# Kernel tuning notes

Hardware: AMD Instinct MI355X
Metric: run time of the kernel (lower is better)

The kernel has to match this reference:

```python
import jax, jax.numpy as jnp
import numpy as np

N = 100000   # num_nodes
D = 128      # hidden_dim
E = 640000   # num_edges


def setup_inputs() -> dict:
    key = jax.random.key(0)
    k0, k1, k2, k3 = jax.random.split(key, 4)
    node_features = jax.random.normal(k0, (N, D), dtype=jnp.float32) * 0.02
    # GCNConv linear weights (glorot-style scale), bias initialized to zero
    scale = 1.0 / np.sqrt(D)
    W1 = jax.random.normal(k1, (D, D), dtype=jnp.float32) * scale
    b1 = jnp.zeros((D,), dtype=jnp.float32)
    W2 = jax.random.normal(k2, (D, D), dtype=jnp.float32) * scale
    b2 = jnp.zeros((D,), dtype=jnp.float32)
    edge_index = jax.random.randint(k3, (2, E), 0, N, dtype=jnp.int32)
    return {"node_features": node_features, "W1": W1, "b1": b1,
            "W2": W2, "b2": b2, "edge_index": edge_index}


def gcn_layer(x, W, b, row, col):
    # PyG GCNConv: linear (no bias) -> symmetric norm deg^-1/2 -> scatter-add -> +bias
    x = x @ W.T                                   # [N, D]
    ones = jnp.ones(row.shape, dtype=x.dtype)
    deg = jax.ops.segment_sum(ones, col, num_segments=N)   # in-degree incl. self-loops
    dis = jnp.where(deg > 0, jax.lax.rsqrt(deg), 0.0)       # deg_inv_sqrt, inf -> 0
    norm = dis[row] * dis[col]                    # [E_tot]
    msgs = norm[:, None] * x[row]                 # gather + scale, [E_tot, D]
    out = jax.ops.segment_sum(msgs, col, num_segments=N)    # scatter-aggregate
    return out + b


def reference(node_features, W1, b1, W2, b2, edge_index):
    # add self-loops once (GCNConv does this per call; same result since graph is static)
    loops = jnp.arange(N, dtype=edge_index.dtype)
    row = jnp.concatenate([edge_index[0], loops])
    col = jnp.concatenate([edge_index[1], loops])
    x = jax.nn.relu(gcn_layer(node_features, W1, b1, row, col))
    x = jax.nn.relu(gcn_layer(x, W2, b2, row, col))
    return x
```

## Files before the change

### kernel.cpp

```cpp
#include <hip/hip_runtime.h>

#define DD 128

typedef short bf16x8 __attribute__((ext_vector_type(8)));
typedef float f32x4 __attribute__((ext_vector_type(4)));

__device__ __forceinline__ unsigned short f2bf(float f) {
    unsigned int u = __builtin_bit_cast(unsigned int, f);
    u += 0x7fffu + ((u >> 16) & 1u);
    return (unsigned short)(u >> 16);
}
__device__ __forceinline__ float bflo(unsigned int u) { return __builtin_bit_cast(float, u << 16); }
__device__ __forceinline__ float bfhi(unsigned int u) { return __builtin_bit_cast(float, u & 0xffff0000u); }

__global__ __launch_bounds__(256) void k_part(const int* __restrict__ cnt,
                                              int* __restrict__ part, int n) {
    __shared__ int s[256];
    int t = threadIdx.x;
    int i = blockIdx.x * 256 + t;
    s[t] = (i < n) ? cnt[i] : 0;
    __syncthreads();
    for (int off = 128; off > 0; off >>= 1) {
        if (t < off) s[t] += s[t + off];
        __syncthreads();
    }
    if (t == 0) part[blockIdx.x] = s[0];
}

__global__ __launch_bounds__(1024) void k_scanpart(int* __restrict__ part, int nblk) {
    __shared__ int s[1024];
    int t = threadIdx.x;
    int v = (t < nblk) ? part[t] : 0;
    s[t] = v;
    __syncthreads();
    for (int off = 1; off < 1024; off <<= 1) {
        int u = (t >= off) ? s[t - off] : 0;
        __syncthreads();
        s[t] += u;
        __syncthreads();
    }
    if (t < nblk) part[t] = s[t] - v;
}

__global__ __launch_bounds__(256) void k_apply(const int* __restrict__ cnt,
                                               const int* __restrict__ part,
                                               int* __restrict__ rowptr,
                                               int* __restrict__ cursor,
                                               float* __restrict__ dis, int n) {
    __shared__ int s[256];
    int t = threadIdx.x;
    int i = blockIdx.x * 256 + t;
    int c = (i < n) ? cnt[i] : 0;
    s[t] = c;
    __syncthreads();
    for (int off = 1; off < 256; off <<= 1) {
        int u = (t >= off) ? s[t - off] : 0;
        __syncthreads();
        s[t] += u;
        __syncthreads();
    }
    int base = part[blockIdx.x] + s[t] - c;
    if (i < n) {
        rowptr[i] = base;
        cursor[i] = base;
        dis[i] = rsqrtf((float)c + 1.0f);
        if (i == n - 1) rowptr[n] = base + c;
    }
}

__global__ void k_permute(const int* __restrict__ row, const int* __restrict__ col,
                          int* __restrict__ cursor, int* __restrict__ srow, int E) {
    int e = blockIdx.x * blockDim.x + threadIdx.x;
    if (e >= E) return;
    int p = atomicAdd(&cursor[col[e]], 1);
    srow[p] = row[e];
}

template <bool INBF16, bool FUSE_COUNT>
__global__ __launch_bounds__(256) void k_gemm_mfma(const void* __restrict__ Xv,
                                                   const float* __restrict__ W,
                                                   unsigned short* __restrict__ Y,
                                                   int nrows, int gemm_blocks,
                                                   const int* __restrict__ col,
                                                   int* __restrict__ cnt, int E) {
    __shared__ unsigned short Ws[128 * 128];
    const int t = threadIdx.x;

    if (FUSE_COUNT && blockIdx.x >= gemm_blocks) {
        int e = (blockIdx.x - gemm_blocks) * 256 + t;
        if (e < E) atomicAdd(&cnt[col[e]], 1);
        return;
    }

    #pragma unroll
    for (int i = 0; i < 8; ++i) {
        int g   = i * 256 + t;
        int row = g >> 4, ch = g & 15;
        const float* src = W + row * 128 + ch * 8;
        float4 f0 = *(const float4*)src;
        float4 f1 = *(const float4*)(src + 4);
        unsigned short u[8] = { f2bf(f0.x), f2bf(f0.y), f2bf(f0.z), f2bf(f0.w),
                                f2bf(f1.x), f2bf(f1.y), f2bf(f1.z), f2bf(f1.w) };
        int dst = row * 128 + ((ch ^ (row & 15)) << 3);
        *(uint4*)&Ws[dst] = *(const uint4*)u;
    }
    __syncthreads();

    const int wid  = t >> 6;
    const int lane = t & 63;
    const int lr   = lane & 15;
    const int lk   = lane >> 4;
    const long r0  = (long)blockIdx.x * 64 + wid * 16;

    long arow = r0 + lr;
    if (arow >= nrows) arow = nrows - 1;

    f32x4 acc[8] = {};

    #pragma unroll
    for (int kc = 0; kc < 4; ++kc) {
        bf16x8 af;
        if (INBF16) {
            const unsigned short* ap = (const unsigned short*)Xv + arow * 128 + kc * 32 + lk * 8;
            af = *(const bf16x8*)ap;
        } else {
            const float* ap = (const float*)Xv + arow * 128 + kc * 32 + lk * 8;
            float4 a0 = *(const float4*)ap;
            float4 a1 = *(const float4*)(ap + 4);
            af[0] = (short)f2bf(a0.x); af[1] = (short)f2bf(a0.y);
            af[2] = (short)f2bf(a0.z); af[3] = (short)f2bf(a0.w);
            af[4] = (short)f2bf(a1.x); af[5] = (short)f2bf(a1.y);
            af[6] = (short)f2bf(a1.z); af[7] = (short)f2bf(a1.w);
        }
        #pragma unroll
        for (int jt = 0; jt < 8; ++jt) {
            int j  = jt * 16 + lr;
            int ch = (kc * 4 + lk) ^ lr;
            const bf16x8* bp = (const bf16x8*)&Ws[j * 128 + (ch << 3)];
            acc[jt] = __builtin_amdgcn_mfma_f32_16x16x32_bf16(af, *bp, acc[jt], 0, 0, 0);
        }
    }

    #pragma unroll
    for (int jt = 0; jt < 8; ++jt) {
        #pragma unroll
        for (int r = 0; r < 4; ++r) {
            long m = r0 + lk * 4 + r;
            if (m < nrows) Y[m * 128 + jt * 16 + lr] = f2bf(acc[jt][r]);
        }
    }
}

__device__ __forceinline__ void fma8(float* acc, float nm, uint4 q) {
    acc[0] += nm * bflo(q.x); acc[1] += nm * bfhi(q.x);
    acc[2] += nm * bflo(q.y); acc[3] += nm * bfhi(q.y);
    acc[4] += nm * bflo(q.z); acc[5] += nm * bfhi(q.z);
    acc[6] += nm * bflo(q.w); acc[7] += nm * bfhi(q.w);
}

template <bool OUTBF16>
__global__ __launch_bounds__(256) void k_agg(const int* __restrict__ rowptr,
                                             const int* __restrict__ srow,
                                             const float* __restrict__ dis,
                                             const unsigned short* __restrict__ xw,
                                             const float* __restrict__ b,
                                             void* __restrict__ outv, int n) {
    int v = blockIdx.x * 16 + (threadIdx.x >> 4);
    if (v >= n) return;
    int c = (threadIdx.x & 15) * 8;

    float dv = dis[v], s = dv * dv;
    float acc[8] = {};
    fma8(acc, s, *(const uint4*)(xw + (long)v * 128 + c));

    int e0 = rowptr[v], e1 = rowptr[v + 1];
    int e = e0;
    for (; e + 2 <= e1; e += 2) {
        int   r1 = srow[e],  r2 = srow[e + 1];
        float n1 = dis[r1] * dv, n2 = dis[r2] * dv;
        uint4 q1 = *(const uint4*)(xw + (long)r1 * 128 + c);
        uint4 q2 = *(const uint4*)(xw + (long)r2 * 128 + c);
        fma8(acc, n1, q1);
        fma8(acc, n2, q2);
    }
    if (e < e1) {
        int   r1 = srow[e];
        float n1 = dis[r1] * dv;
        fma8(acc, n1, *(const uint4*)(xw + (long)r1 * 128 + c));
    }

    float4 b0 = *(const float4*)(b + c);
    float4 b1 = *(const float4*)(b + c + 4);
    float o[8];
    o[0] = fmaxf(acc[0] + b0.x, 0.0f); o[1] = fmaxf(acc[1] + b0.y, 0.0f);
    o[2] = fmaxf(acc[2] + b0.z, 0.0f); o[3] = fmaxf(acc[3] + b0.w, 0.0f);
    o[4] = fmaxf(acc[4] + b1.x, 0.0f); o[5] = fmaxf(acc[5] + b1.y, 0.0f);
    o[6] = fmaxf(acc[6] + b1.z, 0.0f); o[7] = fmaxf(acc[7] + b1.w, 0.0f);

    if (OUTBF16) {
        unsigned int p[4];
        p[0] = (unsigned int)f2bf(o[0]) | ((unsigned int)f2bf(o[1]) << 16);
        p[1] = (unsigned int)f2bf(o[2]) | ((unsigned int)f2bf(o[3]) << 16);
        p[2] = (unsigned int)f2bf(o[4]) | ((unsigned int)f2bf(o[5]) << 16);
        p[3] = (unsigned int)f2bf(o[6]) | ((unsigned int)f2bf(o[7]) << 16);
        *(uint4*)((unsigned short*)outv + (long)v * 128 + c) = *(const uint4*)p;
    } else {
        float* op = (float*)outv + (long)v * 128 + c;
        *(float4*)op       = make_float4(o[0], o[1], o[2], o[3]);
        *(float4*)(op + 4) = make_float4(o[4], o[5], o[6], o[7]);
    }
}

extern "C" void kernel_launch(void* const* d_in, const int* in_sizes, int n_in,
                              void* d_out, int out_size, void* d_ws, size_t ws_size,
                              hipStream_t stream) {
    const float* X  = (const float*)d_in[0];
    const float* W1 = (const float*)d_in[1];
    const float* b1 = (const float*)d_in[2];
    const float* W2 = (const float*)d_in[3];
    const float* b2 = (const float*)d_in[4];
    const int*   ei = (const int*)d_in[5];
    const int N = in_sizes[0] / DD;
    const int E = in_sizes[5] / 2;
    const int* row = ei;
    const int* col = ei + E;

    char* p = (char*)d_ws;
    auto carve = [&](size_t bytes) { char* q = p; p += (bytes + 255) & ~(size_t)255; return q; };
    int*            cnt    = (int*)           carve((size_t)N * 4);
    int*            rowptr = (int*)           carve((size_t)(N + 1) * 4);
    int*            cursor = (int*)           carve((size_t)N * 4);
    int*            part   = (int*)           carve(1024 * 4);
    int*            srow   = (int*)           carve((size_t)E * 4);
    float*          dis    = (float*)         carve((size_t)N * 4);
    unsigned short* xw     = (unsigned short*)carve((size_t)N * DD * 2);
    unsigned short* h1     = (unsigned short*)d_out;

    const int B = 256;
    const int NBLK = (N + 255) / 256;
    const int gemm_grid  = (N + 63) / 64;
    const int count_grid = (E + B - 1) / B;
    const int agg_grid   = (N + 15) / 16;

    hipMemsetAsync(cnt, 0, (size_t)N * 4, stream);
    k_gemm_mfma<false, true><<<gemm_grid + count_grid, B, 0, stream>>>(
        X, W1, xw, N, gemm_grid, col, cnt, E);

    k_part<<<NBLK, B, 0, stream>>>(cnt, part, N);
    k_scanpart<<<1, 1024, 0, stream>>>(part, NBLK);
    k_apply<<<NBLK, B, 0, stream>>>(cnt, part, rowptr, cursor, dis, N);
    k_permute<<<count_grid, B, 0, stream>>>(row, col, cursor, srow, E);

    k_agg<true><<<agg_grid, B, 0, stream>>>(rowptr, srow, dis, xw, b1, h1, N);

    k_gemm_mfma<true, false><<<gemm_grid, B, 0, stream>>>(
        h1, W2, xw, N, gemm_grid, nullptr, nullptr, 0);
    k_agg<false><<<agg_grid, B, 0, stream>>>(rowptr, srow, dis, xw, b2, d_out, N);
}
```

Before: 175.3 us.

## Enlarge GEMM blocks, swap MFMA operands for vector stores, unroll aggregation by four

The GEMM kernel now runs 512 threads per block covering 128 rows, so the bf16 conversion of W into shared memory is spread over more rows. The MFMA operands are swapped so each lane holds four consecutive output columns of a single row, which lets the epilogue write packed 8-byte stores instead of scattered 2-byte stores. The aggregation loop is unrolled to four edges to keep more gathers in flight, with a scalar loop for the remainder. Larger blocks can cut occupancy, and the extra registers from the unroll may limit waves.

```diff
diff --git a/kernel.cpp b/kernel.cpp
--- a/kernel.cpp
+++ b/kernel.cpp
@@ -77,7 +77,7 @@
 }
 
 template <bool INBF16, bool FUSE_COUNT>
-__global__ __launch_bounds__(256) void k_gemm_mfma(const void* __restrict__ Xv,
+__global__ __launch_bounds__(512) void k_gemm_mfma(const void* __restrict__ Xv,
                                                    const float* __restrict__ W,
                                                    unsigned short* __restrict__ Y,
                                                    int nrows, int gemm_blocks,
@@ -87,14 +87,14 @@
     const int t = threadIdx.x;
 
     if (FUSE_COUNT && blockIdx.x >= gemm_blocks) {
-        int e = (blockIdx.x - gemm_blocks) * 256 + t;
+        int e = (blockIdx.x - gemm_blocks) * 512 + t;
         if (e < E) atomicAdd(&cnt[col[e]], 1);
         return;
     }
 
     #pragma unroll
-    for (int i = 0; i < 8; ++i) {
-        int g   = i * 256 + t;
+    for (int i = 0; i < 4; ++i) {
+        int g   = i * 512 + t;
         int row = g >> 4, ch = g & 15;
         const float* src = W + row * 128 + ch * 8;
         float4 f0 = *(const float4*)src;
@@ -110,10 +110,11 @@
     const int lane = t & 63;
     const int lr   = lane & 15;
     const int lk   = lane >> 4;
-    const long r0  = (long)blockIdx.x * 64 + wid * 16;
+    const long r0  = (long)blockIdx.x * 128 + wid * 16;
 
     long arow = r0 + lr;
-    if (arow >= nrows) arow = nrows - 1;
+    bool rowok = arow < nrows;
+    if (!rowok) arow = nrows - 1;
 
     f32x4 acc[8] = {};
 
@@ -137,16 +138,18 @@
             int j  = jt * 16 + lr;
             int ch = (kc * 4 + lk) ^ lr;
             const bf16x8* bp = (const bf16x8*)&Ws[j * 128 + (ch << 3)];
-            acc[jt] = __builtin_amdgcn_mfma_f32_16x16x32_bf16(af, *bp, acc[jt], 0, 0, 0);
+            acc[jt] = __builtin_amdgcn_mfma_f32_16x16x32_bf16(*bp, af, acc[jt], 0, 0, 0);
         }
     }
 
-    #pragma unroll
-    for (int jt = 0; jt < 8; ++jt) {
+    if (rowok) {
+        unsigned short* yp = Y + arow * 128 + lk * 4;
         #pragma unroll
-        for (int r = 0; r < 4; ++r) {
-            long m = r0 + lk * 4 + r;
-            if (m < nrows) Y[m * 128 + jt * 16 + lr] = f2bf(acc[jt][r]);
+        for (int jt = 0; jt < 8; ++jt) {
+            unsigned int d0 = (unsigned int)f2bf(acc[jt][0]) | ((unsigned int)f2bf(acc[jt][1]) << 16);
+            unsigned int d1 = (unsigned int)f2bf(acc[jt][2]) | ((unsigned int)f2bf(acc[jt][3]) << 16);
+            uint2 u; u.x = d0; u.y = d1;
+            *(uint2*)(yp + jt * 16) = u;
         }
     }
 }
@@ -175,15 +178,21 @@
 
     int e0 = rowptr[v], e1 = rowptr[v + 1];
     int e = e0;
-    for (; e + 2 <= e1; e += 2) {
-        int   r1 = srow[e],  r2 = srow[e + 1];
+    for (; e + 4 <= e1; e += 4) {
+        int   r1 = srow[e],     r2 = srow[e + 1];
+        int   r3 = srow[e + 2], r4 = srow[e + 3];
         float n1 = dis[r1] * dv, n2 = dis[r2] * dv;
+        float n3 = dis[r3] * dv, n4 = dis[r4] * dv;
         uint4 q1 = *(const uint4*)(xw + (long)r1 * 128 + c);
         uint4 q2 = *(const uint4*)(xw + (long)r2 * 128 + c);
+        uint4 q3 = *(const uint4*)(xw + (long)r3 * 128 + c);
+        uint4 q4 = *(const uint4*)(xw + (long)r4 * 128 + c);
         fma8(acc, n1, q1);
         fma8(acc, n2, q2);
-    }
-    if (e < e1) {
+        fma8(acc, n3, q3);
+        fma8(acc, n4, q4);
+    }
+    for (; e < e1; ++e) {
         int   r1 = srow[e];
         float n1 = dis[r1] * dv;
         fma8(acc, n1, *(const uint4*)(xw + (long)r1 * 128 + c));
@@ -236,24 +245,24 @@
     unsigned short* xw     = (unsigned short*)carve((size_t)N * DD * 2);
     unsigned short* h1     = (unsigned short*)d_out;
 
-    const int B = 256;
     const int NBLK = (N + 255) / 256;
-    const int gemm_grid  = (N + 63) / 64;
-    const int count_grid = (E + B - 1) / B;
+    const int gemm_grid  = (N + 127) / 128;
+    const int count_grid = (E + 511) / 512;
+    const int perm_grid  = (E + 255) / 256;
     const int agg_grid   = (N + 15) / 16;
 
     hipMemsetAsync(cnt, 0, (size_t)N * 4, stream);
-    k_gemm_mfma<false, true><<<gemm_grid + count_grid, B, 0, stream>>>(
+    k_gemm_mfma<false, true><<<gemm_grid + count_grid, 512, 0, stream>>>(
         X, W1, xw, N, gemm_grid, col, cnt, E);
 
-    k_part<<<NBLK, B, 0, stream>>>(cnt, part, N);
+    k_part<<<NBLK, 256, 0, stream>>>(cnt, part, N);
     k_scanpart<<<1, 1024, 0, stream>>>(part, NBLK);
-    k_apply<<<NBLK, B, 0, stream>>>(cnt, part, rowptr, cursor, dis, N);
-    k_permute<<<count_grid, B, 0, stream>>>(row, col, cursor, srow, E);
-
-    k_agg<true><<<agg_grid, B, 0, stream>>>(rowptr, srow, dis, xw, b1, h1, N);
-
-    k_gemm_mfma<true, false><<<gemm_grid, B, 0, stream>>>(
+    k_apply<<<NBLK, 256, 0, stream>>>(cnt, part, rowptr, cursor, dis, N);
+    k_permute<<<perm_grid, 256, 0, stream>>>(row, col, cursor, srow, E);
+
+    k_agg<true><<<agg_grid, 256, 0, stream>>>(rowptr, srow, dis, xw, b1, h1, N);
+
+    k_gemm_mfma<true, false><<<gemm_grid, 512, 0, stream>>>(
         h1, W2, xw, N, gemm_grid, nullptr, nullptr, 0);
-    k_agg<false><<<agg_grid, B, 0, stream>>>(rowptr, srow, dis, xw, b2, d_out, N);
-}
+    k_agg<false><<<agg_grid, 256, 0, stream>>>(rowptr, srow, dis, xw, b2, d_out, N);
+}
```

After: 174.4 us. About the same (-0.5%).
